# Kernel optimization log

Measured on AMD Instinct MI355X. Metric: run time of the kernel, lower is better.

## Reference

```python
import jax, jax.numpy as jnp
import numpy as np

N_NODES = 50000
N_RAND_EDGES = 1600000  # avg degree ~32
D_IN = 64
D_OUT = 64


def setup_inputs() -> dict:
    key = jax.random.key(0)
    k1, k2, k3, k4, k5 = jax.random.split(key, 5)
    h = jax.random.normal(k1, (N_NODES, D_IN), dtype=jnp.float32)
    # glorot-like scale for the kernel
    kernel = jax.random.normal(k2, (D_IN, D_OUT), dtype=jnp.float32) * (2.0 / (D_IN + D_OUT)) ** 0.5
    bias = jax.random.normal(k3, (D_OUT,), dtype=jnp.float32) * 0.01
    src_r = jax.random.randint(k4, (N_RAND_EDGES,), 0, N_NODES, dtype=jnp.int64 if jax.config.jax_enable_x64 else jnp.int32)
    dst_r = jax.random.randint(k5, (N_RAND_EDGES,), 0, N_NODES, dtype=src_r.dtype)
    loops = jnp.arange(N_NODES, dtype=src_r.dtype)  # add_self_loop, guarantees out_degree > 0
    src = jnp.concatenate([src_r, loops])
    dst = jnp.concatenate([dst_r, loops])
    return {"h": h, "kernel": kernel, "bias": bias, "src": src, "dst": dst}


def reference(h, kernel, bias, src, dst):
    n = h.shape[0]
    # update_all(copy_u('h','m'), sum('m','h')): scatter-sum src features into dst
    agg = jax.ops.segment_sum(h[src], dst, num_segments=n)  # [N, D_IN]
    # norm = out_degrees ** -0.5 (out-degree = edges with node as source)
    deg = jax.ops.segment_sum(jnp.ones(src.shape, dtype=h.dtype), src, num_segments=n)
    norm = deg ** -0.5  # [N]
    # uno: activation(h @ kernel * norm + bias)
    return jax.nn.relu(agg @ kernel * norm[:, None] + bias)
```

## Files before the change

kernel.cpp:

```cpp
#include <hip/hip_runtime.h>

#define D 64
#define BSHIFT 7
#define NPB 128
#define NBMAX 512
#define CAP 8192
#define CAP2 8192
#define A_TILE 4096
#define ECAP CAP
#define EPT (ECAP / 512)
#define ZPAD 2
#define SENT 0xFFFFFFFFu

__device__ __forceinline__ unsigned short f2bf(float f) {
    unsigned int u = __float_as_uint(f);
    u += 0x7FFFu + ((u >> 16) & 1u);
    return (unsigned short)(u >> 16);
}
__device__ __forceinline__ float bflo(unsigned int w) {
    return __uint_as_float(w << 16);
}
__device__ __forceinline__ float bfhi(unsigned int w) {
    return __uint_as_float(w & 0xFFFF0000u);
}

__global__ __launch_bounds__(512) void zero_head_kernel(int* __restrict__ z, int n) {
    int i = blockIdx.x * 512 + threadIdx.x;
    if (i < n) z[i] = 0;
}

__global__ __launch_bounds__(512) void prep_hw_kernel(
    const float* __restrict__ h, const float* __restrict__ W,
    unsigned short* __restrict__ hw,
    int* __restrict__ z1, int zc1, int* __restrict__ z2, int zc2,
    int n_nodes) {
    int t = threadIdx.x;
    int gid = blockIdx.x * 512 + t;
    for (int i = gid; i < zc1; i += gridDim.x * 512) z1[i] = 0;
    for (int i = gid; i < zc2; i += gridDim.x * 512) z2[i] = 0;
    int S = n_nodes + ZPAD;
    if (gid < 16) {
        ((unsigned int*)hw)[(size_t)n_nodes * 16 + gid] = 0u;
    } else if (gid < 32) {
        ((unsigned int*)hw)[(size_t)S * 16 + (size_t)n_nodes * 16 + (gid - 16)] = 0u;
    }
    int lane = t & 63;
    int wv = __builtin_amdgcn_readfirstlane(t >> 6);
    float wcol[D];
    #pragma unroll
    for (int k = 0; k < D; ++k) wcol[k] = W[k * D + lane];
    unsigned short* half0 = hw;
    unsigned short* half1 = hw + (size_t)S * 32;
    int row0 = (blockIdx.x * 8 + wv) * 4;
    if (row0 >= n_nodes) return;
    const float4* hr = (const float4*)(h + (size_t)row0 * D);
    float a0a = 0.f, a0b = 0.f, a1a = 0.f, a1b = 0.f;
    float a2a = 0.f, a2b = 0.f, a3a = 0.f, a3b = 0.f;
    if (row0 + 4 <= n_nodes) {
        #pragma unroll
        for (int k4 = 0; k4 < 16; ++k4) {
            float4 v0 = hr[k4];
            float4 v1 = hr[16 + k4];
            float4 v2 = hr[32 + k4];
            float4 v3 = hr[48 + k4];
            a0a = fmaf(v0.x, wcol[4*k4+0], a0a); a0b = fmaf(v0.y, wcol[4*k4+1], a0b);
            a0a = fmaf(v0.z, wcol[4*k4+2], a0a); a0b = fmaf(v0.w, wcol[4*k4+3], a0b);
            a1a = fmaf(v1.x, wcol[4*k4+0], a1a); a1b = fmaf(v1.y, wcol[4*k4+1], a1b);
            a1a = fmaf(v1.z, wcol[4*k4+2], a1a); a1b = fmaf(v1.w, wcol[4*k4+3], a1b);
            a2a = fmaf(v2.x, wcol[4*k4+0], a2a); a2b = fmaf(v2.y, wcol[4*k4+1], a2b);
            a2a = fmaf(v2.z, wcol[4*k4+2], a2a); a2b = fmaf(v2.w, wcol[4*k4+3], a2b);
            a3a = fmaf(v3.x, wcol[4*k4+0], a3a); a3b = fmaf(v3.y, wcol[4*k4+1], a3b);
            a3a = fmaf(v3.z, wcol[4*k4+2], a3a); a3b = fmaf(v3.w, wcol[4*k4+3], a3b);
        }
        unsigned short r0 = f2bf(a0a + a0b);
        unsigned short r1 = f2bf(a1a + a1b);
        unsigned short r2 = f2bf(a2a + a2b);
        unsigned short r3 = f2bf(a3a + a3b);
        if (lane < 32) {
            half0[(size_t)(row0 + 0) * 32 + lane] = r0;
            half0[(size_t)(row0 + 1) * 32 + lane] = r1;
            half0[(size_t)(row0 + 2) * 32 + lane] = r2;
            half0[(size_t)(row0 + 3) * 32 + lane] = r3;
        } else {
            half1[(size_t)(row0 + 0) * 32 + lane - 32] = r0;
            half1[(size_t)(row0 + 1) * 32 + lane - 32] = r1;
            half1[(size_t)(row0 + 2) * 32 + lane - 32] = r2;
            half1[(size_t)(row0 + 3) * 32 + lane - 32] = r3;
        }
    } else {
        for (int r = 0; r < 4; ++r) {
            int row = row0 + r;
            if (row >= n_nodes) break;
            float aa = 0.f, ab = 0.f;
            #pragma unroll
            for (int k4 = 0; k4 < 16; ++k4) {
                float4 v = hr[r * 16 + k4];
                aa = fmaf(v.x, wcol[4*k4+0], aa); ab = fmaf(v.y, wcol[4*k4+1], ab);
                aa = fmaf(v.z, wcol[4*k4+2], aa); ab = fmaf(v.w, wcol[4*k4+3], ab);
            }
            unsigned short val = f2bf(aa + ab);
            if (lane < 32) half0[(size_t)row * 32 + lane] = val;
            else           half1[(size_t)row * 32 + lane - 32] = val;
        }
    }
}

__global__ __launch_bounds__(512) void partition_kernel(
    const int* __restrict__ src, const int* __restrict__ dst,
    int* __restrict__ hs, int* __restrict__ gcursor, int* __restrict__ gcursor2,
    unsigned int* __restrict__ gp_main, unsigned int* __restrict__ gp_last,
    unsigned short* __restrict__ srcpk,
    int* __restrict__ ofl_cnt, unsigned int* __restrict__ ofl, int ofl_cap,
    int* __restrict__ ofl2_cnt, unsigned int* __restrict__ ofl2, int ofl2_cap,
    int nb, int n_edges, int degmode) {
    __shared__ int lcnt[NBMAX], lbase[NBMAX], lcur[NBMAX], lgres[NBMAX];
    __shared__ int mcnt[NBMAX], mbase[NBMAX], mcur[NBMAX], mgres[NBMAX];
    __shared__ unsigned int sbuf[A_TILE];
    __shared__ unsigned short sbuf2[A_TILE];
    __shared__ int ltot, mtot;
    int t = threadIdx.x;
    int tile = blockIdx.x * A_TILE;

    lcnt[t] = 0; mcnt[t] = 0;
    if (t == 0) { ltot = 0; mtot = 0; }

    int s[8], d[8];
    int e0 = tile + t * 8;
    #pragma unroll
    for (int j = 0; j < 2; ++j) {
        int e = e0 + j * 4;
        if (e + 3 < n_edges) {
            int4 sv = *(const int4*)(src + e);
            int4 dv = *(const int4*)(dst + e);
            s[j*4+0] = sv.x; s[j*4+1] = sv.y; s[j*4+2] = sv.z; s[j*4+3] = sv.w;
            d[j*4+0] = dv.x; d[j*4+1] = dv.y; d[j*4+2] = dv.z; d[j*4+3] = dv.w;
        } else {
            #pragma unroll
            for (int k = 0; k < 4; ++k) {
                int ee = e + k;
                s[j*4+k] = (ee < n_edges) ? src[ee] : -1;
                d[j*4+k] = (ee < n_edges) ? dst[ee] : -1;
            }
        }
    }
    __syncthreads();
    #pragma unroll
    for (int j = 0; j < 8; ++j) {
        if (d[j] >= 0) {
            atomicAdd(&lcnt[d[j] >> BSHIFT], 1);
            if (degmode == 1) atomicAdd(&mcnt[s[j] >> BSHIFT], 1);
            else              atomicAdd(&hs[s[j]], 1);
        }
    }
    __syncthreads();
    int c  = lcnt[t];
    int c2 = mcnt[t];
    int rc  = (c  + 15) & ~15;
    int rc2 = (c2 + 15) & ~15;
    int gr = 0, gr2 = 0;
    if (c  > 0) gr  = atomicAdd(&gcursor[t],  rc);
    if (c2 > 0) gr2 = atomicAdd(&gcursor2[t], rc2);
    int lb  = (c  > 0) ? atomicAdd(&ltot, c)  : 0;
    int lb2 = (c2 > 0) ? atomicAdd(&mtot, c2) : 0;
    lbase[t] = lb;  lcur[t] = lb;
    mbase[t] = lb2; mcur[t] = lb2;
    __syncthreads();
    #pragma unroll
    for (int j = 0; j < 8; ++j) {
        if (d[j] >= 0) {
            int bin = d[j] >> BSHIFT;
            int pos = atomicAdd(&lcur[bin], 1);
            sbuf[pos] = ((unsigned int)d[j] << 16) | (unsigned int)s[j];
            if (degmode == 1) {
                int sbin = s[j] >> BSHIFT;
                int pos2 = atomicAdd(&mcur[sbin], 1);
                sbuf2[pos2] = (unsigned short)s[j];
            }
        }
    }
    lgres[t] = gr; mgres[t] = gr2;
    __syncthreads();
    int m = ltot;
    for (int pos = t; pos < m; pos += 512) {
        unsigned int p = sbuf[pos];
        int bin = (int)(p >> (16 + BSHIFT));
        int gidx = lgres[bin] + (pos - lbase[bin]);
        if (gidx < CAP) {
            unsigned int* gp = (bin == nb - 1) ? gp_last : (gp_main + (size_t)bin * CAP);
            gp[gidx] = p;
        } else {
            int op = atomicAdd(ofl_cnt, 1);
            if (op < ofl_cap) ofl[op] = p;
        }
    }
    int m2 = mtot;
    for (int pos = t; pos < m2; pos += 512) {
        unsigned short v = sbuf2[pos];
        int bin = (int)(v >> BSHIFT);
        int gidx = mgres[bin] + (pos - mbase[bin]);
        if (gidx < CAP2) {
            srcpk[(size_t)bin * CAP2 + gidx] = v;
        } else {
            int op = atomicAdd(ofl2_cnt, 1);
            if (op < ofl2_cap) ofl2[op] = (unsigned int)v;
        }
    }
    for (int i = c; i < rc; ++i) {
        int g = gr + i;
        if (g < CAP) {
            unsigned int* gp = (t == nb - 1) ? gp_last : (gp_main + (size_t)t * CAP);
            gp[g] = SENT;
        }
    }
    for (int i = c2; i < rc2; ++i) {
        int g = gr2 + i;
        if (g < CAP2) srcpk[(size_t)t * CAP2 + g] = 0xFFFFu;
    }
}

__global__ __launch_bounds__(512) void fused_prep_part_kernel(
    const float* __restrict__ h, const float* __restrict__ W,
    unsigned short* __restrict__ hw, int n_nodes,
    const int* __restrict__ src, const int* __restrict__ dst,
    int* __restrict__ gcursor, int* __restrict__ gcursor2,
    unsigned int* __restrict__ gp_main, unsigned int* __restrict__ gp_last,
    unsigned short* __restrict__ srcpk,
    int* __restrict__ ofl_cnt, unsigned int* __restrict__ ofl, int ofl_cap,
    int* __restrict__ ofl2_cnt, unsigned int* __restrict__ ofl2, int ofl2_cap,
    int nb, int n_edges, int ab, int grid_total) {
    __shared__ int lcnt[NBMAX], lbase[NBMAX], lcur[NBMAX], lgres[NBMAX];
    __shared__ int mcnt[NBMAX], mbase[NBMAX], mcur[NBMAX], mgres[NBMAX];
    __shared__ unsigned int sbuf[A_TILE];
    __shared__ unsigned short sbuf2[A_TILE];
    __shared__ int ltot, mtot;
    int t = threadIdx.x;
    int bid = blockIdx.x;
    int q0 = (int)(((long long)bid * ab) / grid_total);
    int q1 = (int)(((long long)(bid + 1) * ab) / grid_total);
    if (q1 > q0) {
        int tile = q0 * A_TILE;
        lcnt[t] = 0; mcnt[t] = 0;
        if (t == 0) { ltot = 0; mtot = 0; }
        int s[8], d[8];
        int e0 = tile + t * 8;
        #pragma unroll
        for (int j = 0; j < 2; ++j) {
            int e = e0 + j * 4;
            if (e + 3 < n_edges) {
                int4 sv = *(const int4*)(src + e);
                int4 dv = *(const int4*)(dst + e);
                s[j*4+0] = sv.x; s[j*4+1] = sv.y; s[j*4+2] = sv.z; s[j*4+3] = sv.w;
                d[j*4+0] = dv.x; d[j*4+1] = dv.y; d[j*4+2] = dv.z; d[j*4+3] = dv.w;
            } else {
                #pragma unroll
                for (int k = 0; k < 4; ++k) {
                    int ee = e + k;
                    s[j*4+k] = (ee < n_edges) ? src[ee] : -1;
                    d[j*4+k] = (ee < n_edges) ? dst[ee] : -1;
                }
            }
        }
        __syncthreads();
        #pragma unroll
        for (int j = 0; j < 8; ++j) {
            if (d[j] >= 0) {
                atomicAdd(&lcnt[d[j] >> BSHIFT], 1);
                atomicAdd(&mcnt[s[j] >> BSHIFT], 1);
            }
        }
        __syncthreads();
        int c  = lcnt[t];
        int c2 = mcnt[t];
        int rc  = (c  + 15) & ~15;
        int rc2 = (c2 + 15) & ~15;
        int gr = 0, gr2 = 0;
        if (c  > 0) gr  = atomicAdd(&gcursor[t],  rc);
        if (c2 > 0) gr2 = atomicAdd(&gcursor2[t], rc2);
        int lb  = (c  > 0) ? atomicAdd(&ltot, c)  : 0;
        int lb2 = (c2 > 0) ? atomicAdd(&mtot, c2) : 0;
        lbase[t] = lb;  lcur[t] = lb;
        mbase[t] = lb2; mcur[t] = lb2;
        __syncthreads();
        #pragma unroll
        for (int j = 0; j < 8; ++j) {
            if (d[j] >= 0) {
                int bin = d[j] >> BSHIFT;
                int pos = atomicAdd(&lcur[bin], 1);
                sbuf[pos] = ((unsigned int)d[j] << 16) | (unsigned int)s[j];
                int sbin = s[j] >> BSHIFT;
                int pos2 = atomicAdd(&mcur[sbin], 1);
                sbuf2[pos2] = (unsigned short)s[j];
            }
        }
        lgres[t] = gr; mgres[t] = gr2;
        __syncthreads();
        int m = ltot;
        for (int pos = t; pos < m; pos += 512) {
            unsigned int p = sbuf[pos];
            int bin = (int)(p >> (16 + BSHIFT));
            int gidx = lgres[bin] + (pos - lbase[bin]);
            if (gidx < CAP) {
                unsigned int* gp = (bin == nb - 1) ? gp_last : (gp_main + (size_t)bin * CAP);
                gp[gidx] = p;
            } else {
                int op = atomicAdd(ofl_cnt, 1);
                if (op < ofl_cap) ofl[op] = p;
            }
        }
        int m2 = mtot;
        for (int pos = t; pos < m2; pos += 512) {
            unsigned short v = sbuf2[pos];
            int bin = (int)(v >> BSHIFT);
            int gidx = mgres[bin] + (pos - mbase[bin]);
            if (gidx < CAP2) {
                srcpk[(size_t)bin * CAP2 + gidx] = v;
            } else {
                int op = atomicAdd(ofl2_cnt, 1);
                if (op < ofl2_cap) ofl2[op] = (unsigned int)v;
            }
        }
        for (int i = c; i < rc; ++i) {
            int g = gr + i;
            if (g < CAP) {
                unsigned int* gp = (t == nb - 1) ? gp_last : (gp_main + (size_t)t * CAP);
                gp[g] = SENT;
            }
        }
        for (int i = c2; i < rc2; ++i) {
            int g = gr2 + i;
            if (g < CAP2) srcpk[(size_t)t * CAP2 + g] = 0xFFFFu;
        }
    } else {
        int prep_idx = bid - q0;
        int gid = prep_idx * 512 + t;
        int S = n_nodes + ZPAD;
        if (gid < 16) {
            ((unsigned int*)hw)[(size_t)n_nodes * 16 + gid] = 0u;
        } else if (gid < 32) {
            ((unsigned int*)hw)[(size_t)S * 16 + (size_t)n_nodes * 16 + (gid - 16)] = 0u;
        }
        int lane = t & 63;
        int wv = __builtin_amdgcn_readfirstlane(t >> 6);
        float wcol[D];
        #pragma unroll
        for (int k = 0; k < D; ++k) wcol[k] = W[k * D + lane];
        unsigned short* half0 = hw;
        unsigned short* half1 = hw + (size_t)S * 32;
        int row0 = (prep_idx * 8 + wv) * 4;
        if (row0 >= n_nodes) return;
        const float4* hr = (const float4*)(h + (size_t)row0 * D);
        float a0a = 0.f, a0b = 0.f, a1a = 0.f, a1b = 0.f;
        float a2a = 0.f, a2b = 0.f, a3a = 0.f, a3b = 0.f;
        if (row0 + 4 <= n_nodes) {
            #pragma unroll
            for (int k4 = 0; k4 < 16; ++k4) {
                float4 v0 = hr[k4];
                float4 v1 = hr[16 + k4];
                float4 v2 = hr[32 + k4];
                float4 v3 = hr[48 + k4];
                a0a = fmaf(v0.x, wcol[4*k4+0], a0a); a0b = fmaf(v0.y, wcol[4*k4+1], a0b);
                a0a = fmaf(v0.z, wcol[4*k4+2], a0a); a0b = fmaf(v0.w, wcol[4*k4+3], a0b);
                a1a = fmaf(v1.x, wcol[4*k4+0], a1a); a1b = fmaf(v1.y, wcol[4*k4+1], a1b);
                a1a = fmaf(v1.z, wcol[4*k4+2], a1a); a1b = fmaf(v1.w, wcol[4*k4+3], a1b);
                a2a = fmaf(v2.x, wcol[4*k4+0], a2a); a2b = fmaf(v2.y, wcol[4*k4+1], a2b);
                a2a = fmaf(v2.z, wcol[4*k4+2], a2a); a2b = fmaf(v2.w, wcol[4*k4+3], a2b);
                a3a = fmaf(v3.x, wcol[4*k4+0], a3a); a3b = fmaf(v3.y, wcol[4*k4+1], a3b);
                a3a = fmaf(v3.z, wcol[4*k4+2], a3a); a3b = fmaf(v3.w, wcol[4*k4+3], a3b);
            }
            unsigned short r0 = f2bf(a0a + a0b);
            unsigned short r1 = f2bf(a1a + a1b);
            unsigned short r2 = f2bf(a2a + a2b);
            unsigned short r3 = f2bf(a3a + a3b);
            if (lane < 32) {
                half0[(size_t)(row0 + 0) * 32 + lane] = r0;
                half0[(size_t)(row0 + 1) * 32 + lane] = r1;
                half0[(size_t)(row0 + 2) * 32 + lane] = r2;
                half0[(size_t)(row0 + 3) * 32 + lane] = r3;
            } else {
                half1[(size_t)(row0 + 0) * 32 + lane - 32] = r0;
                half1[(size_t)(row0 + 1) * 32 + lane - 32] = r1;
                half1[(size_t)(row0 + 2) * 32 + lane - 32] = r2;
                half1[(size_t)(row0 + 3) * 32 + lane - 32] = r3;
            }
        } else {
            for (int r = 0; r < 4; ++r) {
                int row = row0 + r;
                if (row >= n_nodes) break;
                float aa = 0.f, ab2 = 0.f;
                #pragma unroll
                for (int k4 = 0; k4 < 16; ++k4) {
                    float4 v = hr[r * 16 + k4];
                    aa = fmaf(v.x, wcol[4*k4+0], aa); ab2 = fmaf(v.y, wcol[4*k4+1], ab2);
                    aa = fmaf(v.z, wcol[4*k4+2], aa); ab2 = fmaf(v.w, wcol[4*k4+3], ab2);
                }
                unsigned short val = f2bf(aa + ab2);
                if (lane < 32) half0[(size_t)row * 32 + lane] = val;
                else           half1[(size_t)row * 32 + lane - 32] = val;
            }
        }
    }
}

__global__ __launch_bounds__(512) void deg_from_srcpk(
    const int* __restrict__ gcursor2, const unsigned short* __restrict__ srcpk,
    const int* __restrict__ ofl2_cnt_p, const unsigned int* __restrict__ ofl2, int ofl2_cap,
    int* __restrict__ deg, int nb, int n_nodes) {
    __shared__ int hist[NPB];
    int t = threadIdx.x;
    int b = blockIdx.x;
    if (t < NPB) hist[t] = 0;
    __syncthreads();
    int cnt2 = gcursor2[b]; if (cnt2 > CAP2) cnt2 = CAP2;
    const unsigned short* r2 = srcpk + (size_t)b * CAP2;
    for (int i = t; i < cnt2; i += 512) {
        unsigned short v = r2[i];
        if (v != 0xFFFFu) atomicAdd(&hist[v & (NPB - 1)], 1);
    }
    int n2 = *ofl2_cnt_p; if (n2 < 0) n2 = 0; if (n2 > ofl2_cap) n2 = ofl2_cap;
    for (int i = t; i < n2; i += 512) {
        unsigned int v = ofl2[i];
        if ((int)(v >> BSHIFT) == b) atomicAdd(&hist[v & (NPB - 1)], 1);
    }
    __syncthreads();
    if (t < NPB) {
        int node = b * NPB + t;
        if (node < n_nodes) deg[node] = hist[t];
    }
}

__global__ __launch_bounds__(512) void fused_deg_csr_kernel(
    const int* __restrict__ gcursor2, const unsigned short* __restrict__ srcpk,
    const int* __restrict__ ofl2_cnt_p, const unsigned int* __restrict__ ofl2, int ofl2_cap,
    int* __restrict__ deg,
    const int* __restrict__ gcursor,
    const unsigned int* gp_main, const unsigned int* gp_last,
    const int* __restrict__ ofl_cnt_p, const unsigned int* __restrict__ ofl, int ofl_cap,
    unsigned short* __restrict__ gcsr,
    int* __restrict__ nodeoff, int* __restrict__ nodecnt,
    int nb, int n_nodes) {
    __shared__ int hist[NPB];
    __shared__ int lcnt[NPB], loff[NPB], lcur[NPB], lpc[NPB];
    __shared__ unsigned short csr[CAP2];
    int t = threadIdx.x;
    int lane = t & 63;
    int wv = t >> 6;
    int b = blockIdx.x;

    if (t < NPB) { hist[t] = 0; lcnt[t] = 0; }
    __syncthreads();

    int cnt2 = gcursor2[b]; if (cnt2 > CAP2) cnt2 = CAP2;
    const unsigned short* r2 = srcpk + (size_t)b * CAP2;
    for (int i = t; i < cnt2; i += 512) {
        unsigned short v = r2[i];
        if (v != 0xFFFFu) atomicAdd(&hist[v & (NPB - 1)], 1);
    }
    int n2 = *ofl2_cnt_p; if (n2 < 0) n2 = 0; if (n2 > ofl2_cap) n2 = ofl2_cap;
    for (int i = t; i < n2; i += 512) {
        unsigned int v = ofl2[i];
        if ((int)(v >> BSHIFT) == b) atomicAdd(&hist[v & (NPB - 1)], 1);
    }

    const unsigned int* region = (b == nb - 1) ? gp_last : (gp_main + (size_t)b * CAP);
    int cnt = gcursor[b]; if (cnt > CAP) cnt = CAP;
    int ofn = *ofl_cnt_p; if (ofn < 0) ofn = 0; if (ofn > ofl_cap) ofn = ofl_cap;
    unsigned int ep[EPT];
    #pragma unroll
    for (int u = 0; u < EPT; ++u) {
        int i = t + u * 512;
        ep[u] = (i < cnt) ? region[i] : SENT;
    }
    #pragma unroll
    for (int u = 0; u < EPT; ++u) {
        if (ep[u] != SENT && (int)(ep[u] >> (16 + BSHIFT)) == b)
            atomicAdd(&lcnt[(ep[u] >> 16) & (NPB - 1)], 1);
        else ep[u] = SENT;
    }
    for (int i = t; i < ofn; i += 512) {
        unsigned int p = ofl[i];
        if ((int)(p >> (16 + BSHIFT)) == b)
            atomicAdd(&lcnt[(p >> 16) & (NPB - 1)], 1);
    }
    __syncthreads();

    if (t < NPB) {
        int node = b * NPB + t;
        if (node < n_nodes) deg[node] = hist[t];
    }

    if (wv == 0) {
        int c0 = lcnt[lane];
        int c1 = lcnt[lane + 64];
        int p0 = (c0 + 15) & ~15;
        int p1 = (c1 + 15) & ~15;
        int sm = p0 + p1;
        int x = sm;
        #pragma unroll
        for (int o = 1; o < 64; o <<= 1) {
            int y = __shfl_up(x, o);
            if (lane >= o) x += y;
        }
        int base = x - sm;
        loff[lane] = base;            lcur[lane] = base;            lpc[lane] = p0;
        loff[lane + 64] = base + p0;  lcur[lane + 64] = base + p0;  lpc[lane + 64] = p1;
    }
    __syncthreads();
    if (t < NPB) {
        nodeoff[(size_t)b * NPB + t] = loff[t];
        nodecnt[(size_t)b * NPB + t] = lpc[t];
    }
    #pragma unroll
    for (int u = 0; u < EPT; ++u) {
        if (ep[u] != SENT) {
            int nl = (int)((ep[u] >> 16) & (NPB - 1));
            int pos = atomicAdd(&lcur[nl], 1);
            if (pos < CAP2) csr[pos] = (unsigned short)(ep[u] & 0xFFFFu);
        }
    }
    for (int i = t; i < ofn; i += 512) {
        unsigned int p = ofl[i];
        if ((int)(p >> (16 + BSHIFT)) == b) {
            int nl = (int)((p >> 16) & (NPB - 1));
            int pos = atomicAdd(&lcur[nl], 1);
            if (pos < CAP2) csr[pos] = (unsigned short)(p & 0xFFFFu);
        }
    }
    __syncthreads();
    if (t < NPB) {
        int i0 = loff[t] + lcnt[t];
        int i1 = loff[t] + lpc[t];
        for (int i = i0; i < i1; ++i)
            if (i < CAP2) csr[i] = (unsigned short)n_nodes;
    }
    __syncthreads();
    int tot = loff[NPB - 1] + lpc[NPB - 1];
    if (tot > CAP2) tot = CAP2;
    unsigned int* gc = (unsigned int*)(gcsr + (size_t)b * CAP2);
    const unsigned int* lc4 = (const unsigned int*)csr;
    for (int i = t; i < (tot + 1) / 2; i += 512) gc[i] = lc4[i];
}

__global__ __launch_bounds__(512, 2) void gather_csr_kernel(
    const unsigned short* __restrict__ hw, const float* __restrict__ bias,
    const int* __restrict__ degarr,
    const unsigned short* __restrict__ gcsr,
    const int* __restrict__ nodeoff, const int* __restrict__ nodecnt,
    int nb, float* __restrict__ out, int n_nodes, int pass) {
    __shared__ unsigned short csr[CAP2];
    __shared__ int lo[32], lc[32];
    int t = threadIdx.x;
    int lane = t & 63;
    int wv = t >> 6;
    int g = lane >> 3;
    int l8 = lane & 7;
    int blk = blockIdx.x;
    int b = blk >> 2;
    int hh = blk & 3;
    int S = n_nodes + ZPAD;

    int idx0 = b * NPB + hh * 32;
    int base = nodeoff[idx0];
    int end  = nodeoff[idx0 + 31] + nodecnt[idx0 + 31];
    if (base > CAP2) base = CAP2;
    if (end > CAP2) end = CAP2;
    int len = end - base; if (len < 0) len = 0;
    const unsigned int* gc = (const unsigned int*)(gcsr + (size_t)b * CAP2 + base);
    unsigned int* lc4 = (unsigned int*)csr;
    for (int i = t; i < (len + 1) / 2; i += 512) lc4[i] = gc[i];
    if (t < 32) {
        int idx = idx0 + t;
        int off = nodeoff[idx] - base;
        int pc = nodecnt[idx];
        if (off < 0) off = 0;
        if (off > len) off = len;
        if (pc > len - off) pc = (len - off) & ~15;
        if (pc < 0) pc = 0;
        lo[t] = off; lc[t] = pc;
    }
    __syncthreads();

    int pair = wv * 4 + (g >> 1);
    int off = lo[pair];
    int pc = lc[pair];
    float acc[4];
    acc[0] = acc[1] = acc[2] = acc[3] = 0.f;

    const uint2* hwh = (const uint2*)(hw + (size_t)pass * S * 32);
    for (int j = (g & 1) * 8; j < pc; j += 16) {
        uint2 v[8];
        #pragma unroll
        for (int u = 0; u < 8; ++u) {
            int ss = (int)csr[off + j + u];
            v[u] = hwh[(unsigned)(ss * 8 + l8)];
        }
        #pragma unroll
        for (int u = 0; u < 8; ++u) {
            acc[0] += bflo(v[u].x); acc[1] += bfhi(v[u].x);
            acc[2] += bflo(v[u].y); acc[3] += bfhi(v[u].y);
        }
    }

    #pragma unroll
    for (int q = 0; q < 4; ++q)
        acc[q] += __shfl_xor(acc[q], 8);

    if (!(g & 1)) {
        int node = b * NPB + hh * 32 + pair;
        if (node < n_nodes) {
            float4 bv = ((const float4*)bias)[pass * 8 + l8];
            float nrm = rsqrtf((float)degarr[node]);
            float4 r;
            r.x = fmaxf(fmaf(acc[0], nrm, bv.x), 0.f);
            r.y = fmaxf(fmaf(acc[1], nrm, bv.y), 0.f);
            r.z = fmaxf(fmaf(acc[2], nrm, bv.z), 0.f);
            r.w = fmaxf(fmaf(acc[3], nrm, bv.w), 0.f);
            ((float4*)out)[(size_t)node * 16 + pass * 8 + l8] = r;
        }
    }
}

template<int NLOC>
__global__ __launch_bounds__(512, 2) void bucket_gather_t(
    const unsigned short* __restrict__ hw, const float* __restrict__ bias,
    const int* __restrict__ gcursor, const int* __restrict__ degarr,
    const unsigned int* gp_main, const unsigned int* gp_last,
    const int* __restrict__ ofl_cnt_p, const unsigned int* __restrict__ ofl, int ofl_cap,
    int nb, float* out, int n_nodes) {
    constexpr int SPB = NPB / NLOC;
    __shared__ int lcnt[NLOC];
    __shared__ int loff[NLOC];
    __shared__ int lcur[NLOC];
    __shared__ unsigned short csr[ECAP];
    int t = threadIdx.x;
    int lane = t & 63;
    int wv = t >> 6;
    int g = lane >> 3;
    int l8 = lane & 7;
    int blk = blockIdx.x;
    int b = blk / SPB;
    int hh = blk % SPB;
    int S = n_nodes + ZPAD;
    const unsigned int* region = (b == nb - 1) ? gp_last : (gp_main + (size_t)b * CAP);
    int cnt = gcursor[b]; if (cnt > CAP) cnt = CAP;
    int ofn = *ofl_cnt_p; if (ofn < 0) ofn = 0; if (ofn > ofl_cap) ofn = ofl_cap;

    constexpr int KN = NLOC / 64;
    float acc[KN][2][4];
    #pragma unroll
    for (int k = 0; k < KN; ++k)
        #pragma unroll
        for (int p = 0; p < 2; ++p)
            #pragma unroll
            for (int q = 0; q < 4; ++q) acc[k][p][q] = 0.f;

    int nch = 1 + ((ofn > 0) ? (ofn + ECAP - 1) / ECAP : 0);
    for (int ch = 0; ch < nch; ++ch) {
        const unsigned int* sp; int m;
        if (ch == 0) { sp = region; m = cnt; }
        else {
            sp = ofl + (size_t)(ch - 1) * ECAP;
            m = ofn - (ch - 1) * ECAP; if (m > ECAP) m = ECAP;
        }
        if (t < NLOC) lcnt[t] = 0;
        __syncthreads();
        unsigned int ep[EPT];
        #pragma unroll
        for (int u = 0; u < EPT; ++u) {
            int i = t + u * 512;
            ep[u] = (i < m) ? sp[i] : SENT;
        }
        #pragma unroll
        for (int u = 0; u < EPT; ++u) {
            if (ep[u] != SENT) {
                int pb = (int)(ep[u] >> (16 + BSHIFT));
                int nl_r = (int)((ep[u] >> 16) & (NPB - 1));
                if (pb != b || (SPB == 2 && ((nl_r >> 6) != hh))) ep[u] = SENT;
            }
        }
        #pragma unroll
        for (int u = 0; u < EPT; ++u)
            if (ep[u] != SENT)
                atomicAdd(&lcnt[(ep[u] >> 16) & (NLOC - 1)], 1);
        __syncthreads();
        if (wv == 0) {
            if (NLOC == 128) {
                int v0 = lcnt[lane];
                int v1 = lcnt[lane + 64];
                int sm = v0 + v1;
                int x = sm;
                #pragma unroll
                for (int o = 1; o < 64; o <<= 1) {
                    int y = __shfl_up(x, o);
                    if (lane >= o) x += y;
                }
                int base = x - sm;
                loff[lane] = base;            lcur[lane] = base;
                loff[lane + 64] = base + v0;  lcur[lane + 64] = base + v0;
            } else {
                int v = lcnt[lane];
                int x = v;
                #pragma unroll
                for (int o = 1; o < 64; o <<= 1) {
                    int y = __shfl_up(x, o);
                    if (lane >= o) x += y;
                }
                loff[lane] = x - v;
                lcur[lane] = x - v;
            }
        }
        __syncthreads();
        #pragma unroll
        for (int u = 0; u < EPT; ++u)
            if (ep[u] != SENT) {
                int nl = (int)((ep[u] >> 16) & (NLOC - 1));
                int pos = atomicAdd(&lcur[nl], 1);
                csr[pos] = (unsigned short)(ep[u] & 0xFFFFu);
            }
        __syncthreads();
        #pragma unroll
        for (int p = 0; p < 2; ++p) {
            const uint2* hwh = (const uint2*)(hw + (size_t)p * S * 32);
            #pragma unroll
            for (int k = 0; k < KN; ++k) {
                int nl = k * 64 + wv * 8 + g;
                int off = loff[nl];
                int c = lcnt[nl];
                for (int j = 0; j < c; j += 8) {
                    uint2 v[8];
                    bool ok[8];
                    #pragma unroll
                    for (int u = 0; u < 8; ++u) {
                        int idx = j + u;
                        ok[u] = idx < c;
                        int ss = (int)csr[off + (ok[u] ? idx : 0)];
                        v[u] = ok[u] ? hwh[(size_t)ss * 8 + l8] : make_uint2(0, 0);
                    }
                    #pragma unroll
                    for (int u = 0; u < 8; ++u) {
                        acc[k][p][0] += bflo(v[u].x); acc[k][p][1] += bfhi(v[u].x);
                        acc[k][p][2] += bflo(v[u].y); acc[k][p][3] += bfhi(v[u].y);
                    }
                }
            }
        }
        __syncthreads();
    }

    float4 bv0 = ((const float4*)bias)[l8];
    float4 bv1 = ((const float4*)bias)[8 + l8];
    int node0 = b * NPB + hh * 64;
    #pragma unroll
    for (int k = 0; k < KN; ++k) {
        int nl = k * 64 + wv * 8 + g;
        int node = node0 + nl;
        if (node >= n_nodes) continue;
        float nrm = rsqrtf((float)degarr[node]);
        float4 r0, r1;
        r0.x = fmaxf(fmaf(acc[k][0][0], nrm, bv0.x), 0.f);
        r0.y = fmaxf(fmaf(acc[k][0][1], nrm, bv0.y), 0.f);
        r0.z = fmaxf(fmaf(acc[k][0][2], nrm, bv0.z), 0.f);
        r0.w = fmaxf(fmaf(acc[k][0][3], nrm, bv0.w), 0.f);
        r1.x = fmaxf(fmaf(acc[k][1][0], nrm, bv1.x), 0.f);
        r1.y = fmaxf(fmaf(acc[k][1][1], nrm, bv1.y), 0.f);
        r1.z = fmaxf(fmaf(acc[k][1][2], nrm, bv1.z), 0.f);
        r1.w = fmaxf(fmaf(acc[k][1][3], nrm, bv1.w), 0.f);
        ((float4*)out)[(size_t)node * 16 + l8]     = r0;
        ((float4*)out)[(size_t)node * 16 + 8 + l8] = r1;
    }
}


__global__ void deg_kernel(const int* __restrict__ src, float* __restrict__ deg, int n_edges) {
    int e = blockIdx.x * blockDim.x + threadIdx.x;
    if (e < n_edges) atomicAdd(&deg[src[e]], 1.0f);
}

__global__ void scatter_kernel(const float* __restrict__ h, const int* __restrict__ src,
                               const int* __restrict__ dst, float* __restrict__ agg,
                               int n_edges) {
    long long tid = (long long)blockIdx.x * blockDim.x + threadIdx.x;
    int e = (int)(tid >> 6);
    int f = (int)(tid & 63);
    if (e < n_edges) {
        atomicAdd(&agg[(long long)dst[e] * D + f], h[(long long)src[e] * D + f]);
    }
}

__global__ void transform_kernel(float* __restrict__ agg_out, const float* __restrict__ W,
                                 const float* __restrict__ bias, const float* __restrict__ deg,
                                 int n_nodes) {
    __shared__ float w_lds[D][D];
    __shared__ float a_lds[4][D];
    __shared__ float b_lds[D];
    int t = threadIdx.x;
    for (int i = t; i < D * D; i += 256) w_lds[i >> 6][i & 63] = W[i];
    if (t < D) b_lds[t] = bias[t];
    int rl = t >> 6, col = t & 63;
    int row = blockIdx.x * 4 + rl;
    if (row < n_nodes) a_lds[rl][col] = agg_out[(long long)row * D + col];
    __syncthreads();
    if (row < n_nodes) {
        float sum = 0.f;
        #pragma unroll
        for (int k = 0; k < D; ++k) sum = fmaf(a_lds[rl][k], w_lds[k][col], sum);
        float v = fmaf(sum, rsqrtf(deg[row]), b_lds[col]);
        agg_out[(long long)row * D + col] = fmaxf(v, 0.f);
    }
}

extern "C" void kernel_launch(void* const* d_in, const int* in_sizes, int n_in,
                              void* d_out, int out_size, void* d_ws, size_t ws_size,
                              hipStream_t stream) {
    const float* h    = (const float*)d_in[0];
    const float* W    = (const float*)d_in[1];
    const float* bias = (const float*)d_in[2];
    const int*   src  = (const int*)d_in[3];
    const int*   dst  = (const int*)d_in[4];
    float* out = (float*)d_out;

    int n_nodes = in_sizes[0] / D;
    int n_edges = in_sizes[3];
    int nb = (n_nodes + NPB - 1) / NPB;

    bool shape_ok = (nb <= NBMAX - 1) && (n_nodes <= 65408) && (n_nodes % 2 == 0) &&
                    ((size_t)out_size == (size_t)n_nodes * D);
    size_t head = 2 * (size_t)NBMAX + 2;
    size_t hw_ints = (size_t)(n_nodes + ZPAD) * 32;
    size_t gp2   = (head + 3) & ~(size_t)3;
    size_t hw2s  = gp2 + (size_t)nb * CAP;
    size_t spk2  = hw2s + hw_ints;
    size_t csr2  = spk2 + (size_t)nb * (CAP2 / 2);
    size_t ofl2s = csr2 + (size_t)nb * (CAP2 / 2);
    size_t of22s = ofl2s + 16384;
    size_t deg2  = of22s + 8192;
    size_t noff2 = deg2 + n_nodes;
    size_t ncnt2 = noff2 + (size_t)nb * NPB;
    size_t need2 = (ncnt2 + (size_t)nb * NPB) * 4;
    size_t gpl1 = (head + 3) & ~(size_t)3;
    size_t hw1  = gpl1 + CAP;
    size_t spk1 = hw1 + hw_ints;
    size_t ofl1 = spk1 + (size_t)nb * (CAP2 / 2);
    size_t of21 = ofl1 + 16384;
    size_t deg1 = of21 + 8192;
    size_t need1 = (deg1 + n_nodes) * 4;
    size_t hs0  = head;
    size_t gpl0 = (hs0 + n_nodes + 3) & ~(size_t)3;
    size_t hw0  = gpl0 + CAP;
    size_t ofl0 = hw0 + hw_ints;
    size_t need0 = (ofl0 + 16384) * 4;

    if (shape_ok && ws_size >= need0) {
        int mode = (ws_size >= need2) ? 2 : ((ws_size >= need1) ? 1 : 0);
        int* wsI = (int*)d_ws;
        int* gcursor  = wsI;
        int* gcursor2 = wsI + NBMAX;
        int* ofl_cnt  = wsI + 2 * NBMAX;
        int* ofl2_cnt = wsI + 2 * NBMAX + 1;
        unsigned int* gp_main; unsigned int* gp_last;
        unsigned short* hw; unsigned short* srcpk; unsigned short* gcsrp = 0;
        unsigned int* ofl; unsigned int* ofl2;
        int* degp; int* noffp = 0; int* ncntp = 0; int* hs;
        if (mode == 2) {
            gp_main = (unsigned int*)(wsI + gp2);
            gp_last = gp_main + (size_t)(nb - 1) * CAP;
            hw      = (unsigned short*)(wsI + hw2s);
            srcpk   = (unsigned short*)(wsI + spk2);
            gcsrp   = (unsigned short*)(wsI + csr2);
            ofl     = (unsigned int*)(wsI + ofl2s);
            ofl2    = (unsigned int*)(wsI + of22s);
            degp    = wsI + deg2;
            noffp   = wsI + noff2;
            ncntp   = wsI + ncnt2;
            hs      = gcursor;
        } else if (mode == 1) {
            gp_main = (unsigned int*)d_out;
            gp_last = (unsigned int*)(wsI + gpl1);
            hw      = (unsigned short*)(wsI + hw1);
            srcpk   = (unsigned short*)(wsI + spk1);
            ofl     = (unsigned int*)(wsI + ofl1);
            ofl2    = (unsigned int*)(wsI + of21);
            degp    = wsI + deg1;
            hs      = gcursor;
        } else {
            gp_main = (unsigned int*)d_out;
            gp_last = (unsigned int*)(wsI + gpl0);
            hw      = (unsigned short*)(wsI + hw0);
            srcpk   = (unsigned short*)(wsI + gpl0);
            ofl     = (unsigned int*)(wsI + ofl0);
            ofl2    = (unsigned int*)(wsI + ofl0);
            degp    = wsI + hs0;
            hs      = degp;
        }
        int ofl_cap = 16384, ofl2_cap = (mode >= 1) ? 8192 : 0;

        int pb = (n_nodes + 31) / 32;
        int ab = (n_edges + A_TILE - 1) / A_TILE;

        if (mode == 2) {
            zero_head_kernel<<<(int)((head + 511) / 512), 512, 0, stream>>>(wsI, (int)head);
            int grid_total = pb + ab;
            fused_prep_part_kernel<<<grid_total, 512, 0, stream>>>(
                h, W, hw, n_nodes, src, dst, gcursor, gcursor2,
                gp_main, gp_last, srcpk,
                ofl_cnt, ofl, ofl_cap, ofl2_cnt, ofl2, ofl2_cap,
                nb, n_edges, ab, grid_total);
            fused_deg_csr_kernel<<<nb, 512, 0, stream>>>(
                gcursor2, srcpk, ofl2_cnt, ofl2, ofl2_cap, degp,
                gcursor, gp_main, gp_last, ofl_cnt, ofl, ofl_cap,
                gcsrp, noffp, ncntp, nb, n_nodes);
            gather_csr_kernel<<<nb * 4, 512, 0, stream>>>(
                hw, bias, degp, gcsrp, noffp, ncntp, nb, out, n_nodes, 0);
            gather_csr_kernel<<<nb * 4, 512, 0, stream>>>(
                hw, bias, degp, gcsrp, noffp, ncntp, nb, out, n_nodes, 1);
        } else {
            int degmode = (mode >= 1) ? 1 : 0;
            int zc1 = (int)head;
            int zc2 = (mode >= 1) ? 0 : n_nodes;
            int* z2p = (mode >= 1) ? wsI : degp;
            prep_hw_kernel<<<pb, 512, 0, stream>>>(h, W, hw, wsI, zc1, z2p, zc2, n_nodes);
            partition_kernel<<<ab, 512, 0, stream>>>(src, dst, hs, gcursor, gcursor2,
                                                     gp_main, gp_last, srcpk,
                                                     ofl_cnt, ofl, ofl_cap,
                                                     ofl2_cnt, ofl2, ofl2_cap,
                                                     nb, n_edges, degmode);
            if (mode >= 1)
                deg_from_srcpk<<<nb, 512, 0, stream>>>(gcursor2, srcpk, ofl2_cnt, ofl2,
                                                       ofl2_cap, degp, nb, n_nodes);
            bucket_gather_t<128><<<nb, 512, 0, stream>>>(
                hw, bias, gcursor, degp, gp_main, gp_last,
                ofl_cnt, ofl, ofl_cap, nb, out, n_nodes);
        }
    } else {
        float* deg = (float*)d_ws;
        hipMemsetAsync(out, 0, (size_t)n_nodes * D * sizeof(float), stream);
        hipMemsetAsync(deg, 0, (size_t)n_nodes * sizeof(float), stream);
        int eb = (n_edges + 255) / 256;
        deg_kernel<<<eb, 256, 0, stream>>>(src, deg, n_edges);
        long long total = (long long)n_edges * D;
        scatter_kernel<<<(int)((total + 255) / 256), 256, 0, stream>>>(h, src, dst, out, n_edges);
        transform_kernel<<<(n_nodes + 3) / 4, 256, 0, stream>>>(out, W, bias, deg, n_nodes);
    }
}
```

Before: 92.92 us.

## Scatter partitioned edges directly to global and merge two gather passes into one launch

The partition step no longer stages edges in shared-memory buffers for a second coalesced copy-out pass. Each thread now claims a slot in the global bucket cursor and writes its edge straight to the global bucket, which removes about 24KB of LDS, two barriers and the staging loops. The price is scattered, uncoalesced global stores. Separately, the two gather_csr launches (one per half of the feature columns) become a single launch with twice the blocks, each block deriving its pass from its block index, which saves one launch and lets both halves run concurrently.

```diff
diff --git a/kernel.cpp b/kernel.cpp
--- a/kernel.cpp
+++ b/kernel.cpp
@@ -228,11 +228,8 @@
     int* __restrict__ ofl_cnt, unsigned int* __restrict__ ofl, int ofl_cap,
     int* __restrict__ ofl2_cnt, unsigned int* __restrict__ ofl2, int ofl2_cap,
     int nb, int n_edges, int ab, int grid_total) {
-    __shared__ int lcnt[NBMAX], lbase[NBMAX], lcur[NBMAX], lgres[NBMAX];
-    __shared__ int mcnt[NBMAX], mbase[NBMAX], mcur[NBMAX], mgres[NBMAX];
-    __shared__ unsigned int sbuf[A_TILE];
-    __shared__ unsigned short sbuf2[A_TILE];
-    __shared__ int ltot, mtot;
+    __shared__ int lcnt[NBMAX], lcur[NBMAX];
+    __shared__ int mcnt[NBMAX], mcur[NBMAX];
     int t = threadIdx.x;
     int bid = blockIdx.x;
     int q0 = (int)(((long long)bid * ab) / grid_total);
@@ -240,7 +237,6 @@
     if (q1 > q0) {
         int tile = q0 * A_TILE;
         lcnt[t] = 0; mcnt[t] = 0;
-        if (t == 0) { ltot = 0; mtot = 0; }
         int s[8], d[8];
         int e0 = tile + t * 8;
         #pragma unroll
@@ -276,47 +272,30 @@
         int gr = 0, gr2 = 0;
         if (c  > 0) gr  = atomicAdd(&gcursor[t],  rc);
         if (c2 > 0) gr2 = atomicAdd(&gcursor2[t], rc2);
-        int lb  = (c  > 0) ? atomicAdd(&ltot, c)  : 0;
-        int lb2 = (c2 > 0) ? atomicAdd(&mtot, c2) : 0;
-        lbase[t] = lb;  lcur[t] = lb;
-        mbase[t] = lb2; mcur[t] = lb2;
+        lcur[t] = gr;
+        mcur[t] = gr2;
         __syncthreads();
         #pragma unroll
         for (int j = 0; j < 8; ++j) {
             if (d[j] >= 0) {
                 int bin = d[j] >> BSHIFT;
                 int pos = atomicAdd(&lcur[bin], 1);
-                sbuf[pos] = ((unsigned int)d[j] << 16) | (unsigned int)s[j];
+                unsigned int pk = ((unsigned int)d[j] << 16) | (unsigned int)s[j];
+                if (pos < CAP) {
+                    unsigned int* gp = (bin == nb - 1) ? gp_last : (gp_main + (size_t)bin * CAP);
+                    gp[pos] = pk;
+                } else {
+                    int op = atomicAdd(ofl_cnt, 1);
+                    if (op < ofl_cap) ofl[op] = pk;
+                }
                 int sbin = s[j] >> BSHIFT;
                 int pos2 = atomicAdd(&mcur[sbin], 1);
-                sbuf2[pos2] = (unsigned short)s[j];
-            }
-        }
-        lgres[t] = gr; mgres[t] = gr2;
-        __syncthreads();
-        int m = ltot;
-        for (int pos = t; pos < m; pos += 512) {
-            unsigned int p = sbuf[pos];
-            int bin = (int)(p >> (16 + BSHIFT));
-            int gidx = lgres[bin] + (pos - lbase[bin]);
-            if (gidx < CAP) {
-                unsigned int* gp = (bin == nb - 1) ? gp_last : (gp_main + (size_t)bin * CAP);
-                gp[gidx] = p;
-            } else {
-                int op = atomicAdd(ofl_cnt, 1);
-                if (op < ofl_cap) ofl[op] = p;
-            }
-        }
-        int m2 = mtot;
-        for (int pos = t; pos < m2; pos += 512) {
-            unsigned short v = sbuf2[pos];
-            int bin = (int)(v >> BSHIFT);
-            int gidx = mgres[bin] + (pos - mbase[bin]);
-            if (gidx < CAP2) {
-                srcpk[(size_t)bin * CAP2 + gidx] = v;
-            } else {
-                int op = atomicAdd(ofl2_cnt, 1);
-                if (op < ofl2_cap) ofl2[op] = (unsigned int)v;
+                if (pos2 < CAP2) {
+                    srcpk[(size_t)sbin * CAP2 + pos2] = (unsigned short)s[j];
+                } else {
+                    int op = atomicAdd(ofl2_cnt, 1);
+                    if (op < ofl2_cap) ofl2[op] = (unsigned int)s[j];
+                }
             }
         }
         for (int i = c; i < rc; ++i) {
@@ -545,7 +524,7 @@
     const int* __restrict__ degarr,
     const unsigned short* __restrict__ gcsr,
     const int* __restrict__ nodeoff, const int* __restrict__ nodecnt,
-    int nb, float* __restrict__ out, int n_nodes, int pass) {
+    int nb, float* __restrict__ out, int n_nodes) {
     __shared__ unsigned short csr[CAP2];
     __shared__ int lo[32], lc[32];
     int t = threadIdx.x;
@@ -554,8 +533,11 @@
     int g = lane >> 3;
     int l8 = lane & 7;
     int blk = blockIdx.x;
-    int b = blk >> 2;
-    int hh = blk & 3;
+    int half_n = nb * 4;
+    int pass = (blk >= half_n) ? 1 : 0;
+    int r = blk - pass * half_n;
+    int b = r >> 2;
+    int hh = r & 3;
     int S = n_nodes + ZPAD;
 
     int idx0 = b * NPB + hh * 32;
@@ -609,12 +591,12 @@
         if (node < n_nodes) {
             float4 bv = ((const float4*)bias)[pass * 8 + l8];
             float nrm = rsqrtf((float)degarr[node]);
-            float4 r;
-            r.x = fmaxf(fmaf(acc[0], nrm, bv.x), 0.f);
-            r.y = fmaxf(fmaf(acc[1], nrm, bv.y), 0.f);
-            r.z = fmaxf(fmaf(acc[2], nrm, bv.z), 0.f);
-            r.w = fmaxf(fmaf(acc[3], nrm, bv.w), 0.f);
-            ((float4*)out)[(size_t)node * 16 + pass * 8 + l8] = r;
+            float4 rr;
+            rr.x = fmaxf(fmaf(acc[0], nrm, bv.x), 0.f);
+            rr.y = fmaxf(fmaf(acc[1], nrm, bv.y), 0.f);
+            rr.z = fmaxf(fmaf(acc[2], nrm, bv.z), 0.f);
+            rr.w = fmaxf(fmaf(acc[3], nrm, bv.w), 0.f);
+            ((float4*)out)[(size_t)node * 16 + pass * 8 + l8] = rr;
         }
     }
 }
@@ -908,10 +890,8 @@
                 gcursor2, srcpk, ofl2_cnt, ofl2, ofl2_cap, degp,
                 gcursor, gp_main, gp_last, ofl_cnt, ofl, ofl_cap,
                 gcsrp, noffp, ncntp, nb, n_nodes);
-            gather_csr_kernel<<<nb * 4, 512, 0, stream>>>(
-                hw, bias, degp, gcsrp, noffp, ncntp, nb, out, n_nodes, 0);
-            gather_csr_kernel<<<nb * 4, 512, 0, stream>>>(
-                hw, bias, degp, gcsrp, noffp, ncntp, nb, out, n_nodes, 1);
+            gather_csr_kernel<<<nb * 8, 512, 0, stream>>>(
+                hw, bias, degp, gcsrp, noffp, ncntp, nb, out, n_nodes);
         } else {
             int degmode = (mode >= 1) ? 1 : 0;
             int zc1 = (int)head;
```

Result: slower. 97.36 us (+4.8%).
